# Performance work log

Hardware: AMD Instinct MI355X
Metric: run time of the kernel (lower is better)

The kernel has to match this reference:

```python
import jax, jax.numpy as jnp
import numpy as np

NUM_NODES = 100000
RAW_MSG_DIM = 64
MEMORY_DIM = 100
N_ID = 50000
D_MSG = 3 * RAW_MSG_DIM + MEMORY_DIM  # 292
EPS = 1e-5


def _layernorm(x, g, b):
    mu = jnp.mean(x, axis=-1, keepdims=True)
    var = jnp.mean(jnp.square(x - mu), axis=-1, keepdims=True)
    return (x - mu) * jax.lax.rsqrt(var + EPS) * g + b


def setup_inputs() -> dict:
    key = jax.random.key(0)
    ks = jax.random.split(key, 8)
    return {
        "n_id": jnp.arange(N_ID, dtype=jnp.int64) if jax.config.jax_enable_x64 else jnp.arange(N_ID, dtype=jnp.int32),
        "memory": jax.random.normal(ks[0], (NUM_NODES, MEMORY_DIM), jnp.float32),
        "msg_d_store": jax.random.normal(ks[1], (NUM_NODES, RAW_MSG_DIM, 20), jnp.float32),
        "lin_w1": jax.random.normal(ks[2], (10, 20), jnp.float32) * 0.2,
        "lin_b1": jax.random.normal(ks[3], (10,), jnp.float32) * 0.1,
        "lin_w2": jax.random.normal(ks[4], (3, 10), jnp.float32) * 0.2,
        "lin_b2": jax.random.normal(ks[5], (3,), jnp.float32) * 0.1,
        "lin_ln_g": jnp.ones((3,), jnp.float32),
        "lin_ln_b": jnp.zeros((3,), jnp.float32),
        "ln_g": jnp.ones((D_MSG,), jnp.float32),
        "ln_b": jnp.zeros((D_MSG,), jnp.float32),
        "gru_w_ih": jax.random.normal(ks[6], (3 * MEMORY_DIM, D_MSG), jnp.float32) * 0.05,
        "gru_w_hh": jax.random.normal(ks[7], (3 * MEMORY_DIM, MEMORY_DIM), jnp.float32) * 0.05,
    }


def reference(n_id, memory, msg_d_store, lin_w1, lin_b1, lin_w2, lin_b2,
              lin_ln_g, lin_ln_b, ln_g, ln_b, gru_w_ih, gru_w_hh):
    # TGNMemory.__get_updated_memory__. Each node's msg store holds exactly one
    # entry with src == itself, so src_s == src_d == n_id. The scatter
    # msg_perm[assoc[cat(src_s, src_d)]] = cat(msg_s, msg_d) uses torch
    # the msg_d branch affects the output (faithful dead-code elimination).
    mem_n = memory[n_id]                                   # [N, M] irregular gather
    m = msg_d_store[n_id]                                  # [N, R, 20] irregular gather

    # FeedForward(20, 10, 3) with dropout inactive (eval/deterministic)
    h = jax.nn.gelu(jnp.einsum('nrt,ht->nrh', m, lin_w1) + lin_b1, approximate=False)
    y = jnp.einsum('nrh,oh->nro', h, lin_w2) + lin_b2      # [N, R, 3]
    y = _layernorm(y, lin_ln_g, lin_ln_b)
    comp = y.reshape(m.shape[0], -1)                       # [N, 3R]

    msg_perm = jnp.concatenate([mem_n, comp], axis=-1)     # [N, M + 3R]

    # GRUCell (bias=False) on LayerNorm'd message
    x = _layernorm(msg_perm, ln_g, ln_b)
    gi = x @ gru_w_ih.T                                    # [N, 3M]
    gh = mem_n @ gru_w_hh.T                                # [N, 3M]
    gi_r, gi_z, gi_n = jnp.split(gi, 3, axis=-1)
    gh_r, gh_z, gh_n = jnp.split(gh, 3, axis=-1)
    r = jax.nn.sigmoid(gi_r + gh_r)
    z = jax.nn.sigmoid(gi_z + gh_z)
    n = jnp.tanh(gi_n + r * gh_n)
    return (1.0 - z) * n + z * mem_n                       # [N, M]
```

## Files before the change

kernel.cpp:

```cpp
#include <hip/hip_runtime.h>
#include <math.h>

#define TT 20
#define HH 10
#define OO 3
#define MM 100
#define DD 292
#define NPB 4

__device__ __forceinline__ float b2f(unsigned short v){ return __uint_as_float(((unsigned)v)<<16); }
__device__ __forceinline__ float blo(unsigned u){ return __uint_as_float(u<<16); }
__device__ __forceinline__ float bhi(unsigned u){ return __uint_as_float(u & 0xffff0000u); }
__device__ __forceinline__ unsigned short f2b(float f){
    unsigned u=__float_as_uint(f); u += 0x7fffu + ((u>>16)&1u); return (unsigned short)(u>>16);
}

template<bool F32>
__device__ __forceinline__ float ldv(const unsigned short* p, size_t i){
    return F32 ? ((const float*)p)[i] : b2f(p[i]);
}

__global__ void tgn_detect(const unsigned short* __restrict__ mem,
                           const int* __restrict__ nid, int* __restrict__ flags){
    int ln = threadIdx.x;
    unsigned short s = mem[2*ln];
    int e = (s>>7)&0xFF;
    unsigned long long bm = __ballot(e>=100 && e<=140);
    if (ln==0){
        flags[0] = (__popcll(bm) >= 24) ? 0 : 1;
        flags[1] = (nid[1]==0) ? 1 : 0;
    }
}

template<bool F32>
__global__ __launch_bounds__(256) void tgn_main(
    const int* __restrict__ n_id,
    const unsigned short* __restrict__ mem,
    const unsigned short* __restrict__ msg,
    const unsigned short* __restrict__ w1,
    const unsigned short* __restrict__ b1,
    const unsigned short* __restrict__ w2,
    const unsigned short* __restrict__ b2,
    const unsigned short* __restrict__ g3,
    const unsigned short* __restrict__ bb3,
    const unsigned short* __restrict__ lng,
    const unsigned short* __restrict__ lnb,
    const unsigned short* __restrict__ wih,
    const unsigned short* __restrict__ whh,
    void* __restrict__ outv,
    const int* __restrict__ flags)
{
    if (flags[0] != (F32 ? 1 : 0)) return;
    const bool is64 = (flags[1] != 0);

    __shared__ float w1s[HH*TT], w2s[OO*HH];
    __shared__ float b1s[HH], b2s[OO], g3s[OO], b3s[OO];
    __shared__ float lngs[DD], lnbs[DD];
    __shared__ float xs[NPB][DD], ms[NPB][MM];

    const int tid = threadIdx.x;
    for (int i=tid;i<HH*TT;i+=256) w1s[i]=ldv<F32>(w1,i);
    for (int i=tid;i<OO*HH;i+=256) w2s[i]=ldv<F32>(w2,i);
    if (tid<HH) b1s[tid]=ldv<F32>(b1,tid);
    if (tid<OO){ b2s[tid]=ldv<F32>(b2,tid); g3s[tid]=ldv<F32>(g3,tid); b3s[tid]=ldv<F32>(bb3,tid); }
    for (int i=tid;i<DD;i+=256){ lngs[i]=ldv<F32>(lng,i); lnbs[i]=ldv<F32>(lnb,i); }
    __syncthreads();

    const int wv = tid>>6, ln = tid&63;
    const int gidx = blockIdx.x*NPB + wv;
    const int gn = is64 ? (int)((const long long*)n_id)[gidx] : n_id[gidx];

    float mv[TT];
    if (F32){
        const float4* mp = (const float4*)((const float*)msg + (size_t)gn*(64*TT) + ln*TT);
        #pragma unroll
        for (int i=0;i<5;++i){ float4 q=mp[i]; mv[4*i]=q.x; mv[4*i+1]=q.y; mv[4*i+2]=q.z; mv[4*i+3]=q.w; }
    } else {
        const uint2* mp = (const uint2*)(msg + (size_t)gn*(64*TT) + ln*TT);
        #pragma unroll
        for (int i=0;i<5;++i){ uint2 q=mp[i]; mv[4*i]=blo(q.x); mv[4*i+1]=bhi(q.x); mv[4*i+2]=blo(q.y); mv[4*i+3]=bhi(q.y); }
    }
    {
        float h[HH];
        #pragma unroll
        for (int j=0;j<HH;++j){
            float a=b1s[j];
            #pragma unroll
            for (int t=0;t<TT;++t) a += mv[t]*w1s[j*TT+t];
            h[j] = 0.5f*a*(1.0f+erff(a*0.70710678118654752f));
        }
        float y[OO];
        #pragma unroll
        for (int o=0;o<OO;++o){
            float a=b2s[o];
            #pragma unroll
            for (int j=0;j<HH;++j) a += h[j]*w2s[o*HH+j];
            y[o]=a;
        }
        float mu=(y[0]+y[1]+y[2])*(1.0f/3.0f);
        float d0=y[0]-mu, d1=y[1]-mu, d2=y[2]-mu;
        float rs=rsqrtf((d0*d0+d1*d1+d2*d2)*(1.0f/3.0f)+1e-5f);
        xs[wv][MM+3*ln+0]=d0*rs*g3s[0]+b3s[0];
        xs[wv][MM+3*ln+1]=d1*rs*g3s[1]+b3s[1];
        xs[wv][MM+3*ln+2]=d2*rs*g3s[2]+b3s[2];
    }
    for (int i=ln;i<MM;i+=64){
        float v=ldv<F32>(mem,(size_t)gn*MM+i);
        ms[wv][i]=v; xs[wv][i]=v;
    }
    __syncthreads();

    {
        float s=0.f, ss=0.f;
        for (int i=ln;i<DD;i+=64){ float v=xs[wv][i]; s+=v; ss+=v*v; }
        #pragma unroll
        for (int off=32;off>=1;off>>=1){ s+=__shfl_xor(s,off); ss+=__shfl_xor(ss,off); }
        float mu=s*(1.0f/DD);
        float var=ss*(1.0f/DD)-mu*mu;
        float rs=rsqrtf(var+1e-5f);
        for (int i=ln;i<DD;i+=64) xs[wv][i]=(xs[wv][i]-mu)*rs*lngs[i]+lnbs[i];
    }
    __syncthreads();

    for (int jo=ln; jo<MM; jo+=64){
        float ar=0.f,az=0.f,an=0.f;
        if (F32){
            const float4* wr=(const float4*)((const float*)wih + (size_t)jo*DD);
            const float4* wz=(const float4*)((const float*)wih + (size_t)(jo+100)*DD);
            const float4* wn=(const float4*)((const float*)wih + (size_t)(jo+200)*DD);
            for (int c=0;c<DD/4;++c){
                float x0=xs[wv][4*c], x1=xs[wv][4*c+1], x2=xs[wv][4*c+2], x3=xs[wv][4*c+3];
                float4 qr=wr[c], qz=wz[c], qn=wn[c];
                ar += x0*qr.x+x1*qr.y+x2*qr.z+x3*qr.w;
                az += x0*qz.x+x1*qz.y+x2*qz.z+x3*qz.w;
                an += x0*qn.x+x1*qn.y+x2*qn.z+x3*qn.w;
            }
        } else {
            const uint2* wr=(const uint2*)(wih + (size_t)jo*DD);
            const uint2* wz=(const uint2*)(wih + (size_t)(jo+100)*DD);
            const uint2* wn=(const uint2*)(wih + (size_t)(jo+200)*DD);
            for (int c=0;c<DD/4;++c){
                float x0=xs[wv][4*c], x1=xs[wv][4*c+1], x2=xs[wv][4*c+2], x3=xs[wv][4*c+3];
                uint2 qr=wr[c], qz=wz[c], qn=wn[c];
                ar += x0*blo(qr.x)+x1*bhi(qr.x)+x2*blo(qr.y)+x3*bhi(qr.y);
                az += x0*blo(qz.x)+x1*bhi(qz.x)+x2*blo(qz.y)+x3*bhi(qz.y);
                an += x0*blo(qn.x)+x1*bhi(qn.x)+x2*blo(qn.y)+x3*bhi(qn.y);
            }
        }
        float br=0.f,bz=0.f,bn=0.f;
        if (F32){
            const float4* vr=(const float4*)((const float*)whh + (size_t)jo*MM);
            const float4* vz=(const float4*)((const float*)whh + (size_t)(jo+100)*MM);
            const float4* vn=(const float4*)((const float*)whh + (size_t)(jo+200)*MM);
            for (int c=0;c<MM/4;++c){
                float h0=ms[wv][4*c],h1=ms[wv][4*c+1],h2=ms[wv][4*c+2],h3=ms[wv][4*c+3];
                float4 qr=vr[c],qz=vz[c],qn=vn[c];
                br += h0*qr.x+h1*qr.y+h2*qr.z+h3*qr.w;
                bz += h0*qz.x+h1*qz.y+h2*qz.z+h3*qz.w;
                bn += h0*qn.x+h1*qn.y+h2*qn.z+h3*qn.w;
            }
        } else {
            const uint2* vr=(const uint2*)(whh + (size_t)jo*MM);
            const uint2* vz=(const uint2*)(whh + (size_t)(jo+100)*MM);
            const uint2* vn=(const uint2*)(whh + (size_t)(jo+200)*MM);
            for (int c=0;c<MM/4;++c){
                float h0=ms[wv][4*c],h1=ms[wv][4*c+1],h2=ms[wv][4*c+2],h3=ms[wv][4*c+3];
                uint2 qr=vr[c],qz=vz[c],qn=vn[c];
                br += h0*blo(qr.x)+h1*bhi(qr.x)+h2*blo(qr.y)+h3*bhi(qr.y);
                bz += h0*blo(qz.x)+h1*bhi(qz.x)+h2*blo(qz.y)+h3*bhi(qz.y);
                bn += h0*blo(qn.x)+h1*bhi(qn.x)+h2*blo(qn.y)+h3*bhi(qn.y);
            }
        }
        float rg = 1.0f/(1.0f+expf(-(ar+br)));
        float zg = 1.0f/(1.0f+expf(-(az+bz)));
        float ng = tanhf(an + rg*bn);
        float hp = ms[wv][jo];
        float o  = (1.0f-zg)*ng + zg*hp;
        size_t oi = (size_t)gidx*MM + jo;
        if (F32) ((float*)outv)[oi]=o; else ((unsigned short*)outv)[oi]=f2b(o);
    }
}

extern "C" void kernel_launch(void* const* d_in, const int* in_sizes, int n_in,
                              void* d_out, int out_size, void* d_ws, size_t ws_size,
                              hipStream_t stream) {
    (void)in_sizes; (void)n_in; (void)out_size; (void)ws_size;
    const int* n_id           = (const int*)d_in[0];
    const unsigned short* mem = (const unsigned short*)d_in[1];
    const unsigned short* msg = (const unsigned short*)d_in[2];
    const unsigned short* w1  = (const unsigned short*)d_in[3];
    const unsigned short* b1  = (const unsigned short*)d_in[4];
    const unsigned short* w2  = (const unsigned short*)d_in[5];
    const unsigned short* b2  = (const unsigned short*)d_in[6];
    const unsigned short* g3  = (const unsigned short*)d_in[7];
    const unsigned short* bb3 = (const unsigned short*)d_in[8];
    const unsigned short* lng = (const unsigned short*)d_in[9];
    const unsigned short* lnb = (const unsigned short*)d_in[10];
    const unsigned short* wih = (const unsigned short*)d_in[11];
    const unsigned short* whh = (const unsigned short*)d_in[12];
    int* flags = (int*)d_ws;

    tgn_detect<<<1, 64, 0, stream>>>(mem, n_id, flags);

    dim3 grid(50000 / NPB);
    dim3 block(256);
    tgn_main<false><<<grid, block, 0, stream>>>(n_id, mem, msg, w1, b1, w2, b2,
                                                g3, bb3, lng, lnb, wih, whh, d_out, flags);
    tgn_main<true ><<<grid, block, 0, stream>>>(n_id, mem, msg, w1, b1, w2, b2,
                                                g3, bb3, lng, lnb, wih, whh, d_out, flags);
}
```

Before: 2.494 ms.

## Use bf16 MFMA for GRU matmuls with 16-node blocks in bf16 path

Adds a new kernel for the bf16 input path that processes 16 nodes per block and computes the GRU input and hidden projections with 16x16x32 bf16 MFMA instructions. The layernormed message is split into high and low bf16 parts to keep near-fp32 accuracy, and the weights are read straight from global memory as B operands. This replaces the scalar FMA dot products of the old NPB=4 kernel, cutting ALU work and amortising setup over more nodes. The cost is double MFMA work for the split, padding waste on the 100-column and 292-wide dimensions, and extra shared-memory staging.

```diff
diff --git a/kernel.cpp b/kernel.cpp
--- a/kernel.cpp
+++ b/kernel.cpp
@@ -7,6 +7,13 @@
 #define MM 100
 #define DD 292
 #define NPB 4
+#define NB 16
+#define XP 344
+#define MP 136
+
+typedef __attribute__((ext_vector_type(4))) float f32x4;
+typedef __attribute__((ext_vector_type(8))) short s16x8;
+typedef __attribute__((ext_vector_type(4))) short s16x4;
 
 __device__ __forceinline__ float b2f(unsigned short v){ return __uint_as_float(((unsigned)v)<<16); }
 __device__ __forceinline__ float blo(unsigned u){ return __uint_as_float(u<<16); }
@@ -29,6 +36,202 @@
     if (ln==0){
         flags[0] = (__popcll(bm) >= 24) ? 0 : 1;
         flags[1] = (nid[1]==0) ? 1 : 0;
+    }
+}
+
+__global__ __launch_bounds__(256) void tgn_mfma(
+    const int* __restrict__ n_id,
+    const unsigned short* __restrict__ mem,
+    const unsigned short* __restrict__ msg,
+    const unsigned short* __restrict__ w1,
+    const unsigned short* __restrict__ b1,
+    const unsigned short* __restrict__ w2,
+    const unsigned short* __restrict__ b2,
+    const unsigned short* __restrict__ g3,
+    const unsigned short* __restrict__ bb3,
+    const unsigned short* __restrict__ lng,
+    const unsigned short* __restrict__ lnb,
+    const unsigned short* __restrict__ wih,
+    const unsigned short* __restrict__ whh,
+    unsigned short* __restrict__ out,
+    const int* __restrict__ flags)
+{
+    if (flags[0] != 0) return;
+    const bool is64 = (flags[1] != 0);
+
+    __shared__ float w1s[HH*TT], w2s[OO*HH];
+    __shared__ float b1s[HH], b2s[OO], g3s[OO], b3s[OO];
+    __shared__ float lngs[DD], lnbs[DD];
+    __shared__ int   sgn[NB];
+    __shared__ float xsf[NB][DD];
+    __shared__ unsigned short xh[NB][XP];
+    __shared__ unsigned short xl[NB][XP];
+    __shared__ unsigned short msb[NB][MP];
+
+    const int tid = threadIdx.x;
+    for (int i=tid;i<HH*TT;i+=256) w1s[i]=b2f(w1[i]);
+    for (int i=tid;i<OO*HH;i+=256) w2s[i]=b2f(w2[i]);
+    if (tid<HH) b1s[tid]=b2f(b1[tid]);
+    if (tid<OO){ b2s[tid]=b2f(b2[tid]); g3s[tid]=b2f(g3[tid]); b3s[tid]=b2f(bb3[tid]); }
+    for (int i=tid;i<DD;i+=256){ lngs[i]=b2f(lng[i]); lnbs[i]=b2f(lnb[i]); }
+    if (tid<NB){
+        int gp = blockIdx.x*NB + tid;
+        sgn[tid] = is64 ? (int)((const long long*)n_id)[gp] : n_id[gp];
+    }
+    for (int i=tid;i<NB*(320-DD);i+=256){ int r=i/(320-DD), c=DD+(i-r*(320-DD)); xh[r][c]=0; xl[r][c]=0; }
+    for (int i=tid;i<NB*(128-MM);i+=256){ int r=i/(128-MM), c=MM+(i-r*(128-MM)); msb[r][c]=0; }
+    __syncthreads();
+
+    #pragma unroll
+    for (int it=0; it<4; ++it){
+        int rg = tid + 256*it;
+        int nd = rg>>6, rw = rg&63;
+        const uint2* mp = (const uint2*)(msg + (size_t)sgn[nd]*(64*TT) + rw*TT);
+        float mv[TT];
+        #pragma unroll
+        for (int i=0;i<5;++i){ uint2 qq=mp[i]; mv[4*i]=blo(qq.x); mv[4*i+1]=bhi(qq.x); mv[4*i+2]=blo(qq.y); mv[4*i+3]=bhi(qq.y); }
+        float h[HH];
+        #pragma unroll
+        for (int j=0;j<HH;++j){
+            float a=b1s[j];
+            #pragma unroll
+            for (int t=0;t<TT;++t) a += mv[t]*w1s[j*TT+t];
+            h[j] = 0.5f*a*(1.0f+erff(a*0.70710678118654752f));
+        }
+        float y[OO];
+        #pragma unroll
+        for (int o=0;o<OO;++o){
+            float a=b2s[o];
+            #pragma unroll
+            for (int j=0;j<HH;++j) a += h[j]*w2s[o*HH+j];
+            y[o]=a;
+        }
+        float mu=(y[0]+y[1]+y[2])*(1.0f/3.0f);
+        float d0=y[0]-mu, d1=y[1]-mu, d2=y[2]-mu;
+        float rs=rsqrtf((d0*d0+d1*d1+d2*d2)*(1.0f/3.0f)+1e-5f);
+        xsf[nd][MM+3*rw+0]=d0*rs*g3s[0]+b3s[0];
+        xsf[nd][MM+3*rw+1]=d1*rs*g3s[1]+b3s[1];
+        xsf[nd][MM+3*rw+2]=d2*rs*g3s[2]+b3s[2];
+    }
+    for (int i=tid;i<NB*MM;i+=256){
+        int nd=i/MM, c=i-nd*MM;
+        unsigned short v = mem[(size_t)sgn[nd]*MM + c];
+        msb[nd][c]=v;
+        xsf[nd][c]=b2f(v);
+    }
+    __syncthreads();
+
+    const int wv=tid>>6, ln=tid&63;
+    #pragma unroll
+    for (int nn=0;nn<4;++nn){
+        int nd=wv*4+nn;
+        float s=0.f, ss=0.f;
+        for (int i=ln;i<DD;i+=64){ float v=xsf[nd][i]; s+=v; ss+=v*v; }
+        #pragma unroll
+        for (int off=32;off>=1;off>>=1){ s+=__shfl_xor(s,off); ss+=__shfl_xor(ss,off); }
+        float mu=s*(1.0f/DD);
+        float var=ss*(1.0f/DD)-mu*mu;
+        float rs=rsqrtf(var+1e-5f);
+        for (int i=ln;i<DD;i+=64){
+            float v=(xsf[nd][i]-mu)*rs*lngs[i]+lnbs[i];
+            unsigned short hb=f2b(v);
+            xh[nd][i]=hb;
+            xl[nd][i]=f2b(v-b2f(hb));
+        }
+    }
+    __syncthreads();
+
+    const int g=ln>>4, q=ln&15;
+    const f32x4 z4={0.f,0.f,0.f,0.f};
+    for (int tt=wv; tt<7; tt+=4){
+        const int jo  = tt*16+q;
+        const int joc = (jo < MM) ? jo : (MM-1);
+        f32x4 air=z4, aiz=z4, ain=z4;
+        f32x4 ahr=z4, ahz=z4, ahn=z4;
+        const unsigned short* wr  = wih + (size_t)joc*DD;
+        const unsigned short* wzp = wih + (size_t)(joc+MM)*DD;
+        const unsigned short* wnp = wih + (size_t)(joc+2*MM)*DD;
+        #pragma unroll
+        for (int kc=0;kc<9;++kc){
+            const int k0 = kc*32 + g*8;
+            s16x8 ah = *(const s16x8*)&xh[q][k0];
+            s16x8 al = *(const s16x8*)&xl[q][k0];
+            s16x4 r0=*(const s16x4*)(wr +k0), r1=*(const s16x4*)(wr +k0+4);
+            s16x4 z0=*(const s16x4*)(wzp+k0), z1=*(const s16x4*)(wzp+k0+4);
+            s16x4 n0=*(const s16x4*)(wnp+k0), n1=*(const s16x4*)(wnp+k0+4);
+            s16x8 bR=__builtin_shufflevector(r0,r1,0,1,2,3,4,5,6,7);
+            s16x8 bZ=__builtin_shufflevector(z0,z1,0,1,2,3,4,5,6,7);
+            s16x8 bN=__builtin_shufflevector(n0,n1,0,1,2,3,4,5,6,7);
+            air=__builtin_amdgcn_mfma_f32_16x16x32_bf16(ah,bR,air,0,0,0);
+            air=__builtin_amdgcn_mfma_f32_16x16x32_bf16(al,bR,air,0,0,0);
+            aiz=__builtin_amdgcn_mfma_f32_16x16x32_bf16(ah,bZ,aiz,0,0,0);
+            aiz=__builtin_amdgcn_mfma_f32_16x16x32_bf16(al,bZ,aiz,0,0,0);
+            ain=__builtin_amdgcn_mfma_f32_16x16x32_bf16(ah,bN,ain,0,0,0);
+            ain=__builtin_amdgcn_mfma_f32_16x16x32_bf16(al,bN,ain,0,0,0);
+        }
+        {
+            const int k0 = 288 + g*8;
+            s16x8 ah = *(const s16x8*)&xh[q][k0];
+            s16x8 al = *(const s16x8*)&xl[q][k0];
+            s16x4 zv={0,0,0,0};
+            s16x4 r0=*(const s16x4*)(wr +288);
+            s16x4 z0=*(const s16x4*)(wzp+288);
+            s16x4 n0=*(const s16x4*)(wnp+288);
+            if (g){ r0=zv; z0=zv; n0=zv; }
+            s16x8 bR=__builtin_shufflevector(r0,zv,0,1,2,3,4,5,6,7);
+            s16x8 bZ=__builtin_shufflevector(z0,zv,0,1,2,3,4,5,6,7);
+            s16x8 bN=__builtin_shufflevector(n0,zv,0,1,2,3,4,5,6,7);
+            air=__builtin_amdgcn_mfma_f32_16x16x32_bf16(ah,bR,air,0,0,0);
+            air=__builtin_amdgcn_mfma_f32_16x16x32_bf16(al,bR,air,0,0,0);
+            aiz=__builtin_amdgcn_mfma_f32_16x16x32_bf16(ah,bZ,aiz,0,0,0);
+            aiz=__builtin_amdgcn_mfma_f32_16x16x32_bf16(al,bZ,aiz,0,0,0);
+            ain=__builtin_amdgcn_mfma_f32_16x16x32_bf16(ah,bN,ain,0,0,0);
+            ain=__builtin_amdgcn_mfma_f32_16x16x32_bf16(al,bN,ain,0,0,0);
+        }
+        const unsigned short* vr = whh + (size_t)joc*MM;
+        const unsigned short* vz = whh + (size_t)(joc+MM)*MM;
+        const unsigned short* vn = whh + (size_t)(joc+2*MM)*MM;
+        #pragma unroll
+        for (int kc=0;kc<3;++kc){
+            const int k0 = kc*32 + g*8;
+            s16x8 am = *(const s16x8*)&msb[q][k0];
+            s16x4 r0=*(const s16x4*)(vr+k0), r1=*(const s16x4*)(vr+k0+4);
+            s16x4 z0=*(const s16x4*)(vz+k0), z1=*(const s16x4*)(vz+k0+4);
+            s16x4 n0=*(const s16x4*)(vn+k0), n1=*(const s16x4*)(vn+k0+4);
+            s16x8 bR=__builtin_shufflevector(r0,r1,0,1,2,3,4,5,6,7);
+            s16x8 bZ=__builtin_shufflevector(z0,z1,0,1,2,3,4,5,6,7);
+            s16x8 bN=__builtin_shufflevector(n0,n1,0,1,2,3,4,5,6,7);
+            ahr=__builtin_amdgcn_mfma_f32_16x16x32_bf16(am,bR,ahr,0,0,0);
+            ahz=__builtin_amdgcn_mfma_f32_16x16x32_bf16(am,bZ,ahz,0,0,0);
+            ahn=__builtin_amdgcn_mfma_f32_16x16x32_bf16(am,bN,ahn,0,0,0);
+        }
+        {
+            const int k0 = 96 + g*8;
+            s16x8 am = *(const s16x8*)&msb[q][k0];
+            s16x4 zv={0,0,0,0};
+            s16x4 r0=*(const s16x4*)(vr+96);
+            s16x4 z0=*(const s16x4*)(vz+96);
+            s16x4 n0=*(const s16x4*)(vn+96);
+            if (g){ r0=zv; z0=zv; n0=zv; }
+            s16x8 bR=__builtin_shufflevector(r0,zv,0,1,2,3,4,5,6,7);
+            s16x8 bZ=__builtin_shufflevector(z0,zv,0,1,2,3,4,5,6,7);
+            s16x8 bN=__builtin_shufflevector(n0,zv,0,1,2,3,4,5,6,7);
+            ahr=__builtin_amdgcn_mfma_f32_16x16x32_bf16(am,bR,ahr,0,0,0);
+            ahz=__builtin_amdgcn_mfma_f32_16x16x32_bf16(am,bZ,ahz,0,0,0);
+            ahn=__builtin_amdgcn_mfma_f32_16x16x32_bf16(am,bN,ahn,0,0,0);
+        }
+        if (jo < MM){
+            const size_t ob = (size_t)blockIdx.x*NB*MM;
+            #pragma unroll
+            for (int rr2=0; rr2<4; ++rr2){
+                int m = g*4 + rr2;
+                float rgate = 1.f/(1.f+expf(-(air[rr2]+ahr[rr2])));
+                float zgate = 1.f/(1.f+expf(-(aiz[rr2]+ahz[rr2])));
+                float ngate = tanhf(ain[rr2] + rgate*ahn[rr2]);
+                float hp = b2f(msb[m][jo]);
+                out[ob + (size_t)m*MM + jo] = f2b((1.f-zgate)*ngate + zgate*hp);
+            }
+        }
     }
 }
 
@@ -202,10 +405,10 @@
 
     tgn_detect<<<1, 64, 0, stream>>>(mem, n_id, flags);
 
-    dim3 grid(50000 / NPB);
-    dim3 block(256);
-    tgn_main<false><<<grid, block, 0, stream>>>(n_id, mem, msg, w1, b1, w2, b2,
-                                                g3, bb3, lng, lnb, wih, whh, d_out, flags);
-    tgn_main<true ><<<grid, block, 0, stream>>>(n_id, mem, msg, w1, b1, w2, b2,
-                                                g3, bb3, lng, lnb, wih, whh, d_out, flags);
-}
+    tgn_mfma<<<dim3(50000 / NB), dim3(256), 0, stream>>>(
+        n_id, mem, msg, w1, b1, w2, b2, g3, bb3, lng, lnb, wih, whh,
+        (unsigned short*)d_out, flags);
+
+    tgn_main<true><<<dim3(50000 / NPB), dim3(256), 0, stream>>>(
+        n_id, mem, msg, w1, b1, w2, b2, g3, bb3, lng, lnb, wih, whh, d_out, flags);
+}
```

Result: no change. 2.505 ms (+0.4%).
